# Optimization experiments

Hardware: AMD Instinct MI355X
Metric: run time of the kernel (lower is better)

## Reference

```python
import jax, jax.numpy as jnp
import numpy as np

NUM_CLASSES = 1000
BRANCH = 10


def _build_parent(num_classes=NUM_CLASSES, branch=BRANCH):
    """Balanced hierarchy: leaves 0..C-1, internal nodes appended level by level.
    Returns (parent dict node->parent or None, total node count)."""
    parent = {}
    level = list(range(num_classes))
    nxt = num_classes
    while len(level) > 1:
        new = []
        for s in range(0, len(level), branch):
            p = nxt
            nxt += 1
            for c in level[s:s + branch]:
                parent[c] = p
            new.append(p)
        level = new
    parent[level[0]] = None
    return parent, nxt


def _build_matrices():
    parent, n_nodes = _build_parent()
    C = NUM_CLASSES
    # A[l, n] = 1 if n is l or an ancestor of l  (so probs = outputs @ A)
    A = np.zeros((C, n_nodes), dtype=np.float32)
    Wt = np.zeros((C, n_nodes), dtype=np.float32)
    for l in range(C):
        node = l
        A[l, node] = 1.0
        while parent[node] is not None:
            node = parent[node]
            A[l, node] = 1.0
    for t in range(C):
        node = t
        path = [node]
        while parent[node] is not None:
            node = parent[node]
            path = [node] + path  # root ... t
        L = len(path)
        for j, n in enumerate(path):
            Wt[t, n] += 2.0 ** (-(j + 1))
        Wt[t, t] += 2.0 ** (-L)  # extra target term in the original code
    return jnp.asarray(A), jnp.asarray(Wt)


_A, _WT = _build_matrices()


def setup_inputs() -> dict:
    key = jax.random.key(0)
    k1, k2 = jax.random.split(key)
    B = 32768
    outputs = jax.random.normal(k1, (B, NUM_CLASSES), dtype=jnp.float32)
    target = jax.random.randint(k2, (B,), 0, NUM_CLASSES, dtype=jnp.int64 if jax.config.jax_enable_x64 else jnp.int32)
    return {"outputs": outputs, "target": target}


def reference(outputs, target):
    # probs[i, n] = sum over leaves l of outputs[i, l] where n is ancestor-or-self of l
    probs = outputs @ _A                      # [B, n_nodes]
    w = _WT[target]                           # [B, n_nodes] gathered path weights
    win = jnp.einsum('bn,bn->b', probs, w)    # [B]
    return jnp.sum(1.0 - win)                 # scalar loss
```

## Files before the change

kernel.cpp:

```cpp
#include <hip/hip_runtime.h>


constexpr int C_COLS = 1000;
constexpr int F4_PER_ROW = 250;

__global__ __launch_bounds__(256) void hloss_stage1(
    const float* __restrict__ outputs,
    const int*   __restrict__ target,
    float* __restrict__ partials)
{
    const int wave = threadIdx.x >> 6;
    const int lane = threadIdx.x & 63;
    const int row  = (blockIdx.x << 2) | wave;

    const int t     = target[row];
    const int lo100 = (t / 100) * 100;
    const int lo10  = (t / 10)  * 10;

    const float4* rp = reinterpret_cast<const float4*>(outputs + (size_t)row * C_COLS);

    float tot = 0.f, s100 = 0.f, s10e = 0.f;

#pragma unroll
    for (int k = 0; k < 4; ++k) {
        const int f = (k << 6) + lane;
        if (f < F4_PER_ROW) {
            const float4 v = rp[f];
            const int c = f << 2;
            const float e[4] = {v.x, v.y, v.z, v.w};
#pragma unroll
            for (int j = 0; j < 4; ++j) {
                const int   cc = c + j;
                const float ee = e[j];
                tot  += ee;
                s100 += (cc >= lo100 && cc < lo100 + 100) ? ee : 0.f;
                s10e += (cc >= lo10  && cc < lo10  + 10 ) ? ee : 0.f;
                s10e += (cc == t) ? ee : 0.f;
            }
        }
    }

#pragma unroll
    for (int off = 32; off >= 1; off >>= 1) {
        tot  += __shfl_xor(tot,  off, 64);
        s100 += __shfl_xor(s100, off, 64);
        s10e += __shfl_xor(s10e, off, 64);
    }

    __shared__ float part[4];
    if (lane == 0) {
        part[wave] = 0.5f * tot + 0.25f * s100 + 0.125f * s10e;
    }
    __syncthreads();
    if (threadIdx.x == 0) {
        partials[blockIdx.x] = part[0] + part[1] + part[2] + part[3];
    }
}

__global__ __launch_bounds__(256) void hloss_stage2(
    const float* __restrict__ partials,
    float* __restrict__ out,
    int n_f4, float Bf)
{
    const int lane = threadIdx.x & 63;
    const int wave = threadIdx.x >> 6;
    const float4* p = reinterpret_cast<const float4*>(partials);

    float s = 0.f;
    for (int i = threadIdx.x; i < n_f4; i += 256) {
        const float4 v = p[i];
        s += (v.x + v.y) + (v.z + v.w);
    }
#pragma unroll
    for (int off = 32; off >= 1; off >>= 1) {
        s += __shfl_xor(s, off, 64);
    }
    __shared__ float part[4];
    if (lane == 0) part[wave] = s;
    __syncthreads();
    if (threadIdx.x == 0) {
        out[0] = Bf - (part[0] + part[1] + part[2] + part[3]);
    }
}

extern "C" void kernel_launch(void* const* d_in, const int* in_sizes, int n_in,
                              void* d_out, int out_size, void* d_ws, size_t ws_size,
                              hipStream_t stream)
{
    const float* outputs = (const float*)d_in[0];
    const int*   target  = (const int*)d_in[1];
    float*       loss    = (float*)d_out;
    float*       partials = (float*)d_ws;

    const int B = in_sizes[1];
    const int nblocks = B / 4;

    hloss_stage1<<<nblocks, 256, 0, stream>>>(outputs, target, partials);
    hloss_stage2<<<1, 256, 0, stream>>>(partials, loss, nblocks / 4, (float)B);
}
```

Before: 185.8 us.

## Simplify per-row weighting and process two rows per wave

```diff
diff --git a/kernel.cpp b/kernel.cpp
--- a/kernel.cpp
+++ b/kernel.cpp
@@ -2,7 +2,6 @@
 
 
 constexpr int C_COLS = 1000;
-constexpr int F4_PER_ROW = 250;
 
 __global__ __launch_bounds__(256) void hloss_stage1(
     const float* __restrict__ outputs,
@@ -11,49 +10,46 @@
 {
     const int wave = threadIdx.x >> 6;
     const int lane = threadIdx.x & 63;
-    const int row  = (blockIdx.x << 2) | wave;
+    const int row0 = blockIdx.x * 8 + wave * 2;
 
-    const int t     = target[row];
-    const int lo100 = (t / 100) * 100;
-    const int lo10  = (t / 10)  * 10;
-
-    const float4* rp = reinterpret_cast<const float4*>(outputs + (size_t)row * C_COLS);
-
-    float tot = 0.f, s100 = 0.f, s10e = 0.f;
+    float lw = 0.f;
 
 #pragma unroll
-    for (int k = 0; k < 4; ++k) {
-        const int f = (k << 6) + lane;
-        if (f < F4_PER_ROW) {
-            const float4 v = rp[f];
-            const int c = f << 2;
-            const float e[4] = {v.x, v.y, v.z, v.w};
+    for (int r = 0; r < 2; ++r) {
+        const int row  = row0 + r;
+        const int t    = target[row];
+        const int f100 = (t / 100) * 25;
+        const int lo10 = (t / 10) * 10;
+
+        const float*  rowp = outputs + (size_t)row * C_COLS;
+        const float4* rp   = reinterpret_cast<const float4*>(rowp);
+
 #pragma unroll
-            for (int j = 0; j < 4; ++j) {
-                const int   cc = c + j;
-                const float ee = e[j];
-                tot  += ee;
-                s100 += (cc >= lo100 && cc < lo100 + 100) ? ee : 0.f;
-                s10e += (cc >= lo10  && cc < lo10  + 10 ) ? ee : 0.f;
-                s10e += (cc == t) ? ee : 0.f;
+        for (int k = 0; k < 4; ++k) {
+            const int f = (k << 6) + lane;
+            if (f < 250) {
+                const float4 v  = rp[f];
+                const float  s4 = (v.x + v.y) + (v.z + v.w);
+                const float  w  = ((unsigned)(f - f100) < 25u) ? 0.75f : 0.5f;
+                lw = fmaf(s4, w, lw);
             }
+        }
+        if (lane < 11) {
+            const int col = (lane < 10) ? (lo10 + lane) : t;
+            lw = fmaf(0.125f, rowp[col], lw);
         }
     }
 
 #pragma unroll
     for (int off = 32; off >= 1; off >>= 1) {
-        tot  += __shfl_xor(tot,  off, 64);
-        s100 += __shfl_xor(s100, off, 64);
-        s10e += __shfl_xor(s10e, off, 64);
+        lw += __shfl_xor(lw, off, 64);
     }
 
     __shared__ float part[4];
-    if (lane == 0) {
-        part[wave] = 0.5f * tot + 0.25f * s100 + 0.125f * s10e;
-    }
+    if (lane == 0) part[wave] = lw;
     __syncthreads();
     if (threadIdx.x == 0) {
-        partials[blockIdx.x] = part[0] + part[1] + part[2] + part[3];
+        partials[blockIdx.x] = (part[0] + part[1]) + (part[2] + part[3]);
     }
 }
 
@@ -79,7 +75,7 @@
     if (lane == 0) part[wave] = s;
     __syncthreads();
     if (threadIdx.x == 0) {
-        out[0] = Bf - (part[0] + part[1] + part[2] + part[3]);
+        out[0] = Bf - ((part[0] + part[1]) + (part[2] + part[3]));
     }
 }
 
@@ -87,13 +83,13 @@
                               void* d_out, int out_size, void* d_ws, size_t ws_size,
                               hipStream_t stream)
 {
-    const float* outputs = (const float*)d_in[0];
-    const int*   target  = (const int*)d_in[1];
-    float*       loss    = (float*)d_out;
+    const float* outputs  = (const float*)d_in[0];
+    const int*   target   = (const int*)d_in[1];
+    float*       loss     = (float*)d_out;
     float*       partials = (float*)d_ws;
 
     const int B = in_sizes[1];
-    const int nblocks = B / 4;
+    const int nblocks = B / 8;
 
     hloss_stage1<<<nblocks, 256, 0, stream>>>(outputs, target, partials);
     hloss_stage2<<<1, 256, 0, stream>>>(partials, loss, nblocks / 4, (float)B);
```

After: 187.7 us. No clear change (+1.0%).
